# Optimization experiments

Measured on AMD Instinct MI355X. Metric: run time of the kernel, lower is better.

## Reference

```python
import jax, jax.numpy as jnp
import numpy as np

B, P, L = 16, 196, 80
DIM1, DIM2, ATT = 2048, 300, 512
TAU = 1.0


def setup_inputs() -> dict:
    key = jax.random.key(0)
    ks = jax.random.split(key, 8)
    s1 = 1.0 / np.sqrt(DIM1)
    s2 = 1.0 / np.sqrt(DIM2)
    sa = 1.0 / np.sqrt(ATT)
    return {
        "x1": jax.random.normal(ks[0], (B, P, DIM1), dtype=jnp.float32),
        "x2": jax.random.normal(ks[1], (B, L, DIM2), dtype=jnp.float32),
        # nn.Linear weights stored as (out, in), like torch
        "W1": jax.random.uniform(ks[2], (ATT, DIM1), jnp.float32, -s1, s1),
        "W2": jax.random.uniform(ks[3], (ATT, DIM2), jnp.float32, -s2, s2),
        "Wh": jax.random.uniform(ks[4], (ATT, ATT), jnp.float32, -sa, sa),
        "bh": jax.random.uniform(ks[5], (ATT,), jnp.float32, -sa, sa),
        "Wt": jax.random.uniform(ks[6], (1, ATT), jnp.float32, -sa, sa),
        "bt": jax.random.uniform(ks[7], (1,), jnp.float32, -sa, sa),
    }


def reference(x1, x2, W1, W2, Wh, bh, Wt, bt):
    # projections: (B,P,ATT) and (B,L,ATT)
    p1 = jnp.einsum("bpd,ad->bpa", x1, W1)
    p2 = jnp.einsum("bld,ad->bla", x2, W2)
    # broadcast bilinear interaction: (B,L,P,ATT)
    m = jnp.tanh(p1[:, None, :, :] * p2[:, :, None, :])
    h = jnp.einsum("blpa,ca->blpc", m, Wh) + bh
    # score: (B,L,P)
    t = jnp.einsum("blpa,a->blp", h, Wt[0]) + bt[0]
    alpha = jax.nn.softmax(t / TAU, axis=-1)
    # weighted sum over pixels: (B,L,DIM1)
    label_repr = jnp.einsum("blp,bpd->bld", alpha, x1)
    return (label_repr, alpha)
```

## Files before the change

### kernel.cpp

```cpp
#include <hip/hip_runtime.h>

#define B_   16
#define P_   196
#define L_   80
#define DIM1 2048
#define DIM2 300
#define ATT  512

typedef __attribute__((ext_vector_type(8))) short short8x;
typedef __attribute__((ext_vector_type(8))) unsigned short ushort8x;
typedef __attribute__((ext_vector_type(4))) float f32x4;
typedef __attribute__((ext_vector_type(4))) unsigned int uint4x;
typedef __attribute__((ext_vector_type(4))) unsigned short ushort4x;

__device__ __forceinline__ unsigned short f2bf(float f) {
    unsigned v = __float_as_uint(f);
    v += 0x7fffu + ((v >> 16) & 1u);
    return (unsigned short)(v >> 16);
}

__global__ __launch_bounds__(256)
void weff_kernel(const float* __restrict__ Wh, const float* __restrict__ Wt,
                 float* __restrict__ w_eff) {
    __shared__ float part[4][64];
    const int tid = threadIdx.x, lane = tid & 63, quad = tid >> 6;
    const int a = blockIdx.x * 64 + lane;
    float s = 0.f;
    const int c0 = quad * 128;
    for (int c = c0; c < c0 + 128; ++c)
        s = fmaf(Wt[c], Wh[(size_t)c * ATT + a], s);
    part[quad][lane] = s;
    __syncthreads();
    if (tid < 64)
        w_eff[blockIdx.x * 64 + tid] =
            (part[0][tid] + part[1][tid]) + (part[2][tid] + part[3][tid]);
}

__global__ __launch_bounds__(256)
void cvt_bf16_kernel(const float* __restrict__ in, unsigned short* __restrict__ out, int n4) {
    for (int i = blockIdx.x * 256 + threadIdx.x; i < n4; i += gridDim.x * 256) {
        uint4x u = ((const uint4x*)in)[i];
        ushort4x o;
        #pragma unroll
        for (int j = 0; j < 4; ++j) {
            unsigned v = u[j];
            v += 0x7fffu + ((v >> 16) & 1u);
            o[j] = (unsigned short)(v >> 16);
        }
        ((ushort4x*)out)[i] = o;
    }
}

__global__ __launch_bounds__(256)
void gemm_nt(const float* __restrict__ A, const float* __restrict__ Bm,
             float* __restrict__ C, int M, int N, int K) {
    constexpr int BK = 16;
    __shared__ float As[BK][64];
    __shared__ float Bs[BK][64];
    const int tid  = threadIdx.x;
    const int bm   = blockIdx.x * 64;
    const int bn   = blockIdx.y * 64;
    const int ty   = tid >> 4;
    const int tx   = tid & 15;
    const int lrow = tid >> 2;
    const int lc4  = (tid & 3) << 2;
    float acc[4][4] = {};
    const float* Arow = A  + (size_t)(bm + lrow) * K;
    const float* Brow = Bm + (size_t)(bn + lrow) * K;

    for (int k0 = 0; k0 < K; k0 += BK) {
        float4 av, bv;
        if (k0 + BK <= K) {
            av = *(const float4*)(Arow + k0 + lc4);
            bv = *(const float4*)(Brow + k0 + lc4);
        } else {
            float a_[4], b_[4];
            #pragma unroll
            for (int i = 0; i < 4; ++i) {
                const int k = k0 + lc4 + i;
                a_[i] = (k < K) ? Arow[k] : 0.f;
                b_[i] = (k < K) ? Brow[k] : 0.f;
            }
            av = make_float4(a_[0], a_[1], a_[2], a_[3]);
            bv = make_float4(b_[0], b_[1], b_[2], b_[3]);
        }
        __syncthreads();
        As[lc4 + 0][lrow] = av.x;  As[lc4 + 1][lrow] = av.y;
        As[lc4 + 2][lrow] = av.z;  As[lc4 + 3][lrow] = av.w;
        Bs[lc4 + 0][lrow] = bv.x;  Bs[lc4 + 1][lrow] = bv.y;
        Bs[lc4 + 2][lrow] = bv.z;  Bs[lc4 + 3][lrow] = bv.w;
        __syncthreads();
        #pragma unroll
        for (int k = 0; k < BK; ++k) {
            const float4 a4 = *(const float4*)&As[k][ty << 2];
            const float4 b4 = *(const float4*)&Bs[k][tx << 2];
            const float ae[4] = {a4.x, a4.y, a4.z, a4.w};
            const float be[4] = {b4.x, b4.y, b4.z, b4.w};
            #pragma unroll
            for (int i = 0; i < 4; ++i)
                #pragma unroll
                for (int j = 0; j < 4; ++j)
                    acc[i][j] = fmaf(ae[i], be[j], acc[i][j]);
        }
    }
    #pragma unroll
    for (int i = 0; i < 4; ++i) {
        float4 o = make_float4(acc[i][0], acc[i][1], acc[i][2], acc[i][3]);
        *(float4*)(C + (size_t)(bm + (ty << 2) + i) * N + bn + (tx << 2)) = o;
    }
}

#define GM 3136
#define GN 512
#define GK 2048

__device__ __forceinline__ void gload16(const unsigned short* g, unsigned short* l) {
    __builtin_amdgcn_global_load_lds(
        (const __attribute__((address_space(1))) unsigned int*)g,
        (__attribute__((address_space(3))) unsigned int*)l, 16, 0, 0);
}

__global__ __launch_bounds__(256)
void gemm_bf16_mfma(const unsigned short* __restrict__ Ab,
                    const unsigned short* __restrict__ Bb,
                    unsigned short* __restrict__ C) {
    __shared__ unsigned short As[2][64 * 64];
    __shared__ unsigned short Bs[2][32 * 64];
    const int tid  = threadIdx.x;
    const int wid  = tid >> 6;
    const int lane = tid & 63;
    const int bm   = blockIdx.y * 64;
    const int bn   = blockIdx.x * 32;

    const int srow = lane >> 3;
    const int scol = ((lane & 7) ^ srow) << 3;
    const size_t arow0 = (size_t)(bm + (wid << 4) + srow) * GK;
    const size_t brow0 = (size_t)(bn + (wid << 3) + srow) * GK;

#define STAGE_TILE(buf, k0)                                                              \
    {                                                                                    \
        gload16(Ab + arow0 + (k0) + scol,                  &As[buf][((wid << 4) + 0) * 64]); \
        gload16(Ab + arow0 + (size_t)8 * GK + (k0) + scol, &As[buf][((wid << 4) + 8) * 64]); \
        gload16(Bb + brow0 + (k0) + scol,                  &Bs[buf][(wid << 3) * 64]);       \
    }

    f32x4 acc[2] = {};
    const int fr  = lane & 15;
    const int kb  = (lane >> 4) << 3;
    const int swz = (lane & 7) << 4;

    STAGE_TILE(0, 0)
    constexpr int NT = GK / 64;
    for (int kt = 0; kt < NT; ++kt) {
        __syncthreads();
        if (kt + 1 < NT) STAGE_TILE((kt + 1) & 1, (kt + 1) * 64)
        const char* pa = (const char*)&As[kt & 1][0];
        const char* pb = (const char*)&Bs[kt & 1][0];
        #pragma unroll
        for (int kk = 0; kk < 2; ++kk) {
            const int koff = ((kk * 32 + kb) * 2) ^ swz;
            short8x a = *(const short8x*)(pa + ((wid << 4) + fr) * 128 + koff);
            short8x b[2];
            #pragma unroll
            for (int n = 0; n < 2; ++n)
                b[n] = *(const short8x*)(pb + (n * 16 + fr) * 128 + koff);
            #pragma unroll
            for (int n = 0; n < 2; ++n)
                acc[n] = __builtin_amdgcn_mfma_f32_16x16x32_bf16(a, b[n], acc[n], 0, 0, 0);
        }
        __syncthreads();
    }

    const int crow = (lane >> 4) << 2;
    #pragma unroll
    for (int n = 0; n < 2; ++n)
        #pragma unroll
        for (int j = 0; j < 4; ++j)
            C[(size_t)(bm + (wid << 4) + crow + j) * GN + bn + n * 16 + fr] =
                f2bf(acc[n][j]);
#undef STAGE_TILE
}

#define LOG2E2 2.8853900817779268f

__global__ __launch_bounds__(256)
void score_softmax_kernel(const unsigned short* __restrict__ p1,
                          const float* __restrict__ p2,
                          const float* __restrict__ w_eff,
                          float* __restrict__ alpha) {
    const int bidx = blockIdx.x;
    const int bl = (bidx & 7) * 160 + (bidx >> 3);
    const int b  = bl / L_;
    __shared__ float s_t[P_];
    __shared__ float s_red[4];
    const int tid = threadIdx.x, wave = tid >> 6, lane = tid & 63;
    const int g = lane >> 4, c = lane & 15;

    const float4* gp2 = (const float4*)(p2 + (size_t)bl * ATT);
    const float4* gw  = (const float4*)w_eff;
    float qa[4][8], wa[4][8];
    #pragma unroll
    for (int j = 0; j < 4; ++j) {
        const float4 qlo = gp2[32 * j + 2 * c], qhi = gp2[32 * j + 2 * c + 1];
        const float4 wlo = gw[32 * j + 2 * c],  whi = gw[32 * j + 2 * c + 1];
        qa[j][0] = qlo.x * LOG2E2; qa[j][1] = qlo.y * LOG2E2;
        qa[j][2] = qlo.z * LOG2E2; qa[j][3] = qlo.w * LOG2E2;
        qa[j][4] = qhi.x * LOG2E2; qa[j][5] = qhi.y * LOG2E2;
        qa[j][6] = qhi.z * LOG2E2; qa[j][7] = qhi.w * LOG2E2;
        wa[j][0] = wlo.x; wa[j][1] = wlo.y; wa[j][2] = wlo.z; wa[j][3] = wlo.w;
        wa[j][4] = whi.x; wa[j][5] = whi.y; wa[j][6] = whi.z; wa[j][7] = whi.w;
    }

    const unsigned short* p1b = p1 + (size_t)b * P_ * ATT;
    const int nch = (wave == 0) ? 13 : 12;
    const int ptail = 192 + g;
    ushort8x cur[4], nxt[4];
    {
        const int row0 = 4 * wave + g;
        const ushort8x* row = (const ushort8x*)(p1b + (size_t)row0 * ATT);
        #pragma unroll
        for (int j = 0; j < 4; ++j) cur[j] = row[c + 16 * j];
    }
    for (int i = 0; i < nch; ++i) {
        const int pr = (i < 12) ? (16 * i + 4 * wave + g) : ptail;
        if (i + 1 < nch) {
            const int pn = (i + 1 < 12) ? (16 * (i + 1) + 4 * wave + g) : ptail;
            const ushort8x* row = (const ushort8x*)(p1b + (size_t)pn * ATT);
            #pragma unroll
            for (int j = 0; j < 4; ++j) nxt[j] = row[c + 16 * j];
        }
        float acc = 0.f;
        #pragma unroll
        for (int j = 0; j < 4; ++j) {
            float r[8];
            #pragma unroll
            for (int e = 0; e < 8; ++e)
                r[e] = __uint_as_float((unsigned)cur[j][e] << 16);
            #pragma unroll
            for (int pq = 0; pq < 4; ++pq) {
                const float e0 = __builtin_amdgcn_exp2f(r[2 * pq]     * qa[j][2 * pq]);
                const float e1 = __builtin_amdgcn_exp2f(r[2 * pq + 1] * qa[j][2 * pq + 1]);
                const float w0 = wa[j][2 * pq], w1 = wa[j][2 * pq + 1];
                const float num = fmaf(w0, e1, fmaf(w1, e0, w0 + w1));
                const float den = fmaf(e0, e1, e0 + e1 + 1.f);
                acc = fmaf(num, __builtin_amdgcn_rcpf(den), acc);
            }
        }
        acc += __shfl_xor(acc, 1);
        acc += __shfl_xor(acc, 2);
        acc += __shfl_xor(acc, 4);
        acc += __shfl_xor(acc, 8);
        if (c == 0) s_t[pr] = acc;
        #pragma unroll
        for (int j = 0; j < 4; ++j) cur[j] = nxt[j];
    }
    __syncthreads();
    const float v = (tid < P_) ? -2.f * s_t[tid] : -1e30f;
    float m = v;
    #pragma unroll
    for (int off = 32; off >= 1; off >>= 1) m = fmaxf(m, __shfl_xor(m, off));
    if (lane == 0) s_red[wave] = m;
    __syncthreads();
    m = fmaxf(fmaxf(s_red[0], s_red[1]), fmaxf(s_red[2], s_red[3]));
    __syncthreads();
    const float e = (tid < P_) ? __expf(v - m) : 0.f;
    float s = e;
    #pragma unroll
    for (int off = 32; off >= 1; off >>= 1) s += __shfl_xor(s, off);
    if (lane == 0) s_red[wave] = s;
    __syncthreads();
    s = s_red[0] + s_red[1] + s_red[2] + s_red[3];
    if (tid < P_) alpha[(size_t)bl * P_ + tid] = e / s;
}

__global__ __launch_bounds__(256)
void label_kernel(const float* __restrict__ alpha, const float* __restrict__ x1,
                  float* __restrict__ out) {
    const int dt = blockIdx.x;
    const int lt = blockIdx.y;
    const int b  = blockIdx.z;
    const int tid = threadIdx.x;
    const int d = dt * 256 + tid;
    const float* xcol = x1 + (size_t)b * P_ * DIM1 + d;
    const float* arow = alpha + (size_t)(b * L_ + lt * 16) * P_;
    float acc[16] = {};
    for (int p = 0; p < P_; p += 4) {
        const float xv0 = xcol[(size_t)(p + 0) * DIM1];
        const float xv1 = xcol[(size_t)(p + 1) * DIM1];
        const float xv2 = xcol[(size_t)(p + 2) * DIM1];
        const float xv3 = xcol[(size_t)(p + 3) * DIM1];
        #pragma unroll
        for (int i = 0; i < 16; ++i) {
            const float* ap = arow + i * P_ + p;
            acc[i] = fmaf(ap[0], xv0,
                     fmaf(ap[1], xv1,
                     fmaf(ap[2], xv2,
                     fmaf(ap[3], xv3, acc[i]))));
        }
    }
    #pragma unroll
    for (int i = 0; i < 16; ++i)
        out[(size_t)(b * L_ + lt * 16 + i) * DIM1 + d] = acc[i];
}

extern "C" void kernel_launch(void* const* d_in, const int* in_sizes, int n_in,
                              void* d_out, int out_size, void* d_ws, size_t ws_size,
                              hipStream_t stream) {
    const float* x1 = (const float*)d_in[0];
    const float* x2 = (const float*)d_in[1];
    const float* W1 = (const float*)d_in[2];
    const float* W2 = (const float*)d_in[3];
    const float* Wh = (const float*)d_in[4];
    const float* Wt = (const float*)d_in[6];

    char* base = (char*)d_ws;
    unsigned short* p1b = (unsigned short*)base;
    float* p2    = (float*)(base + 3211264);
    float* w_eff = (float*)(base + 3211264 + 2621440);
    unsigned short* x1b = (unsigned short*)(base + 3211264 + 2621440 + 2048);
    unsigned short* W1b = x1b + (size_t)B_ * P_ * DIM1;

    float* label = (float*)d_out;
    float* alpha = label + (size_t)B_ * L_ * DIM1;

    hipLaunchKernelGGL(cvt_bf16_kernel, dim3(2048), dim3(256), 0, stream,
                       x1, x1b, (B_ * P_ * DIM1) / 4);
    hipLaunchKernelGGL(cvt_bf16_kernel, dim3(512), dim3(256), 0, stream,
                       W1, W1b, (ATT * DIM1) / 4);
    hipLaunchKernelGGL(weff_kernel, dim3(8), dim3(256), 0, stream, Wh, Wt, w_eff);
    hipLaunchKernelGGL(gemm_nt, dim3((B_ * L_) / 64, ATT / 64), dim3(256), 0, stream,
                       x2, W2, p2, B_ * L_, ATT, DIM2);
    hipLaunchKernelGGL(gemm_bf16_mfma, dim3(GN / 32, GM / 64), dim3(256), 0, stream,
                       x1b, W1b, p1b);
    hipLaunchKernelGGL(score_softmax_kernel, dim3(B_ * L_), dim3(256), 0, stream,
                       p1b, p2, w_eff, alpha);
    hipLaunchKernelGGL(label_kernel, dim3(8, 5, B_), dim3(256), 0, stream,
                       alpha, x1, label);
}
```

Before: 208.6 us.

## Fuse prep kernels and rework label kernel with bf16 x1 and shared alpha

Merges the two bf16 conversion kernels and the w_eff kernel into one launch with block-range dispatch, removing two launches. The label kernel now reads the bf16 copy of x1 instead of fp32, halving its main memory traffic. It also stages alpha transposed in shared memory and computes a 4x4 register tile per thread with vector loads and stores. The cost is lower precision in the label output, since x1 is rounded to bf16.

```diff
diff --git a/kernel.cpp b/kernel.cpp
--- a/kernel.cpp
+++ b/kernel.cpp
@@ -20,34 +20,51 @@
 }
 
 __global__ __launch_bounds__(256)
-void weff_kernel(const float* __restrict__ Wh, const float* __restrict__ Wt,
+void prep_kernel(const float* __restrict__ x1, const float* __restrict__ W1,
+                 const float* __restrict__ Wh, const float* __restrict__ Wt,
+                 unsigned short* __restrict__ x1b, unsigned short* __restrict__ W1b,
                  float* __restrict__ w_eff) {
     __shared__ float part[4][64];
-    const int tid = threadIdx.x, lane = tid & 63, quad = tid >> 6;
-    const int a = blockIdx.x * 64 + lane;
-    float s = 0.f;
-    const int c0 = quad * 128;
-    for (int c = c0; c < c0 + 128; ++c)
-        s = fmaf(Wt[c], Wh[(size_t)c * ATT + a], s);
-    part[quad][lane] = s;
-    __syncthreads();
-    if (tid < 64)
-        w_eff[blockIdx.x * 64 + tid] =
-            (part[0][tid] + part[1][tid]) + (part[2][tid] + part[3][tid]);
-}
-
-__global__ __launch_bounds__(256)
-void cvt_bf16_kernel(const float* __restrict__ in, unsigned short* __restrict__ out, int n4) {
-    for (int i = blockIdx.x * 256 + threadIdx.x; i < n4; i += gridDim.x * 256) {
-        uint4x u = ((const uint4x*)in)[i];
-        ushort4x o;
-        #pragma unroll
-        for (int j = 0; j < 4; ++j) {
-            unsigned v = u[j];
-            v += 0x7fffu + ((v >> 16) & 1u);
-            o[j] = (unsigned short)(v >> 16);
-        }
-        ((ushort4x*)out)[i] = o;
+    const int blk = blockIdx.x, tid = threadIdx.x;
+    if (blk < 2048) {
+        const int n4 = (B_ * P_ * DIM1) / 4;
+        for (int i = blk * 256 + tid; i < n4; i += 2048 * 256) {
+            uint4x u = ((const uint4x*)x1)[i];
+            ushort4x o;
+            #pragma unroll
+            for (int j = 0; j < 4; ++j) {
+                unsigned v = u[j];
+                v += 0x7fffu + ((v >> 16) & 1u);
+                o[j] = (unsigned short)(v >> 16);
+            }
+            ((ushort4x*)x1b)[i] = o;
+        }
+    } else if (blk < 2560) {
+        const int n4 = (ATT * DIM1) / 4;
+        for (int i = (blk - 2048) * 256 + tid; i < n4; i += 512 * 256) {
+            uint4x u = ((const uint4x*)W1)[i];
+            ushort4x o;
+            #pragma unroll
+            for (int j = 0; j < 4; ++j) {
+                unsigned v = u[j];
+                v += 0x7fffu + ((v >> 16) & 1u);
+                o[j] = (unsigned short)(v >> 16);
+            }
+            ((ushort4x*)W1b)[i] = o;
+        }
+    } else {
+        const int bix = blk - 2560;
+        const int lane = tid & 63, quad = tid >> 6;
+        const int a = bix * 64 + lane;
+        float s = 0.f;
+        const int c0 = quad * 128;
+        for (int c = c0; c < c0 + 128; ++c)
+            s = fmaf(Wt[c], Wh[(size_t)c * ATT + a], s);
+        part[quad][lane] = s;
+        __syncthreads();
+        if (tid < 64)
+            w_eff[bix * 64 + tid] =
+                (part[0][tid] + part[1][tid]) + (part[2][tid] + part[3][tid]);
     }
 }
 
@@ -274,33 +291,45 @@
 }
 
 __global__ __launch_bounds__(256)
-void label_kernel(const float* __restrict__ alpha, const float* __restrict__ x1,
+void label_kernel(const float* __restrict__ alpha, const unsigned short* __restrict__ x1b,
                   float* __restrict__ out) {
-    const int dt = blockIdx.x;
-    const int lt = blockIdx.y;
-    const int b  = blockIdx.z;
+    const int raw = blockIdx.x;
+    const int dt = raw & 7;
+    const int t  = raw >> 3;
+    const int lt = t % 5;
+    const int b  = t / 5;
+    __shared__ float s_alpha[P_][16];
     const int tid = threadIdx.x;
-    const int d = dt * 256 + tid;
-    const float* xcol = x1 + (size_t)b * P_ * DIM1 + d;
-    const float* arow = alpha + (size_t)(b * L_ + lt * 16) * P_;
-    float acc[16] = {};
+    for (int idx = tid; idx < 16 * P_; idx += 256) {
+        const int p = idx >> 4, i = idx & 15;
+        s_alpha[p][i] = alpha[(size_t)(b * L_ + lt * 16 + i) * P_ + p];
+    }
+    __syncthreads();
+    const int ty = tid >> 6, tx = tid & 63;
+    const int d  = dt * 256 + tx * 4;
+    const unsigned short* xp = x1b + (size_t)b * P_ * DIM1 + d;
+    f32x4 acc[4] = {};
     for (int p = 0; p < P_; p += 4) {
-        const float xv0 = xcol[(size_t)(p + 0) * DIM1];
-        const float xv1 = xcol[(size_t)(p + 1) * DIM1];
-        const float xv2 = xcol[(size_t)(p + 2) * DIM1];
-        const float xv3 = xcol[(size_t)(p + 3) * DIM1];
-        #pragma unroll
-        for (int i = 0; i < 16; ++i) {
-            const float* ap = arow + i * P_ + p;
-            acc[i] = fmaf(ap[0], xv0,
-                     fmaf(ap[1], xv1,
-                     fmaf(ap[2], xv2,
-                     fmaf(ap[3], xv3, acc[i]))));
-        }
-    }
-    #pragma unroll
-    for (int i = 0; i < 16; ++i)
-        out[(size_t)(b * L_ + lt * 16 + i) * DIM1 + d] = acc[i];
+        #pragma unroll
+        for (int u = 0; u < 4; ++u) {
+            const ushort4x xv = *(const ushort4x*)(xp + (size_t)(p + u) * DIM1);
+            float xf[4];
+            #pragma unroll
+            for (int j = 0; j < 4; ++j)
+                xf[j] = __uint_as_float((unsigned)xv[j] << 16);
+            const float4 a = *(const float4*)&s_alpha[p + u][ty << 2];
+            const float av[4] = {a.x, a.y, a.z, a.w};
+            #pragma unroll
+            for (int i2 = 0; i2 < 4; ++i2)
+                #pragma unroll
+                for (int j = 0; j < 4; ++j)
+                    acc[i2][j] = fmaf(av[i2], xf[j], acc[i2][j]);
+        }
+    }
+    const int lbase = b * L_ + lt * 16 + (ty << 2);
+    #pragma unroll
+    for (int i2 = 0; i2 < 4; ++i2)
+        *(f32x4*)(out + (size_t)(lbase + i2) * DIM1 + d) = acc[i2];
 }
 
 extern "C" void kernel_launch(void* const* d_in, const int* in_sizes, int n_in,
@@ -323,17 +352,14 @@
     float* label = (float*)d_out;
     float* alpha = label + (size_t)B_ * L_ * DIM1;
 
-    hipLaunchKernelGGL(cvt_bf16_kernel, dim3(2048), dim3(256), 0, stream,
-                       x1, x1b, (B_ * P_ * DIM1) / 4);
-    hipLaunchKernelGGL(cvt_bf16_kernel, dim3(512), dim3(256), 0, stream,
-                       W1, W1b, (ATT * DIM1) / 4);
-    hipLaunchKernelGGL(weff_kernel, dim3(8), dim3(256), 0, stream, Wh, Wt, w_eff);
+    hipLaunchKernelGGL(prep_kernel, dim3(2568), dim3(256), 0, stream,
+                       x1, W1, Wh, Wt, x1b, W1b, w_eff);
     hipLaunchKernelGGL(gemm_nt, dim3((B_ * L_) / 64, ATT / 64), dim3(256), 0, stream,
                        x2, W2, p2, B_ * L_, ATT, DIM2);
     hipLaunchKernelGGL(gemm_bf16_mfma, dim3(GN / 32, GM / 64), dim3(256), 0, stream,
                        x1b, W1b, p1b);
     hipLaunchKernelGGL(score_softmax_kernel, dim3(B_ * L_), dim3(256), 0, stream,
                        p1b, p2, w_eff, alpha);
-    hipLaunchKernelGGL(label_kernel, dim3(8, 5, B_), dim3(256), 0, stream,
-                       alpha, x1, label);
-}
+    hipLaunchKernelGGL(label_kernel, dim3(640), dim3(256), 0, stream,
+                       alpha, x1b, label);
+}
```

Result: faster. 197.2 us (-5.5%).
